# Performance work log

Hardware: AMD Instinct MI355X
Metric: run time of the kernel (lower is better)

## Reference

```python
import jax, jax.numpy as jnp
import numpy as np


def _forward(embed, enc_Wih, enc_Whh, enc_bih, enc_bhh,
             dec_Wih, dec_Whh, dec_bih, dec_bhh,
             qk_W, qk_b, qv_W, qv_b, ak_W, ak_b,
             out_W, out_b, wd_b,
             hfc1_W, hfc1_b, hfc2_W, hfc2_b,
             cfc1_W, cfc1_b, cfc2_W, cfc2_b,
             src_seqs, src_lengths, trg_seqs):
    B, S = src_seqs.shape
    H = enc_Whh.shape[1]

    # ---- encoder LSTM over packed (masked) source ----
    src_embed = embed[src_seqs]                      # [B,S,D]
    xs = jnp.swapaxes(src_embed, 0, 1)               # [S,B,D]
    step_mask = jnp.arange(S)[:, None] < src_lengths[None, :]  # [S,B]

    def enc_step(carry, inp):
        h, c = carry
        x, m = inp
        z = x @ enc_Wih.T + enc_bih + h @ enc_Whh.T + enc_bhh
        i, f, g, o = jnp.split(z, 4, axis=-1)
        c_new = jax.nn.sigmoid(f) * c + jax.nn.sigmoid(i) * jnp.tanh(g)
        h_new = jax.nn.sigmoid(o) * jnp.tanh(c_new)
        m = m[:, None]
        h_new = jnp.where(m, h_new, h)
        c_new = jnp.where(m, c_new, c)
        out = jnp.where(m, h_new, 0.0)               # pad_packed zero-fills
        return (h_new, c_new), out

    h0 = jnp.zeros((B, H), embed.dtype)
    (hT, cT), enc_outs = jax.lax.scan(enc_step, (h0, h0), (xs, step_mask))
    src_hidden = jnp.swapaxes(enc_outs, 0, 1)        # [B,S,H]

    # ---- init_hidden: MLP transforms of final encoder state ----
    dh = jax.nn.relu(hT @ hfc1_W.T + hfc1_b) @ hfc2_W.T + hfc2_b
    dc = jax.nn.relu(cT @ cfc1_W.T + cfc1_b) @ cfc2_W.T + cfc2_b

    # ---- attention keys/values (constant across decode steps) ----
    q_key = jnp.tanh(src_hidden @ qk_W.T + qk_b)     # [B,S,K]
    q_value = src_hidden @ qv_W.T + qv_b             # [B,S,H]
    attn_mask = jnp.arange(S)[None, :] < src_lengths[:, None]  # [B,S]

    # ---- teacher-forced decode loop (sampling_rate = 1.0) ----
    ans_embed = embed[trg_seqs]                      # [B,T,D]
    dec_inputs = jnp.swapaxes(ans_embed[:, :-1, :], 0, 1)  # [T-1,B,D]

    def dec_step(carry, x):
        h, c = carry
        a_key = jnp.tanh(h @ ak_W.T + ak_b)          # [B,K]
        energy = jnp.einsum('bsk,bk->bs', q_key, a_key)
        energy = jnp.where(attn_mask, energy, -jnp.inf)
        w = jax.nn.softmax(energy, axis=1)           # [B,S]
        context = jnp.einsum('bs,bsh->bh', w, q_value)
        xin = jnp.concatenate([x, context], axis=1)  # [B,D+H]
        z = xin @ dec_Wih.T + dec_bih + h @ dec_Whh.T + dec_bhh
        i, f, g, o = jnp.split(z, 4, axis=-1)
        c_new = jax.nn.sigmoid(f) * c + jax.nn.sigmoid(i) * jnp.tanh(g)
        h_new = jax.nn.sigmoid(o) * jnp.tanh(c_new)
        feat = jnp.concatenate([h_new, context], axis=1) @ out_W.T + out_b  # [B,D]
        logits = feat @ embed.T + wd_b               # tied word_dist, [B,V]
        return (h_new, c_new), logits

    _, outs = jax.lax.scan(dec_step, (dh, dc), dec_inputs)  # [T-1,B,V]
    return jnp.swapaxes(outs, 0, 1)                  # [B,T-1,V]


def setup_inputs() -> dict:
    key = jax.random.key(0)
    ks = jax.random.split(key, 30)
    V, D, H, K = 32000, 512, 1024, 100
    B, S, T = 32, 128, 20

    def w(k, shape):
        return jax.random.normal(k, shape, jnp.float32) * 0.05

    inp = {
        'embed': w(ks[0], (V, D)).at[0].set(0.0),  # padding_idx = 0
        'enc_Wih': w(ks[1], (4 * H, D)), 'enc_Whh': w(ks[2], (4 * H, H)),
        'enc_bih': w(ks[3], (4 * H,)).at[H:2 * H].set(0.0),
        'enc_bhh': w(ks[4], (4 * H,)).at[H:2 * H].set(0.0),
        'dec_Wih': w(ks[5], (4 * H, D + H)), 'dec_Whh': w(ks[6], (4 * H, H)),
        'dec_bih': w(ks[7], (4 * H,)).at[H:2 * H].set(0.0),
        'dec_bhh': w(ks[8], (4 * H,)).at[H:2 * H].set(0.0),
        'qk_W': w(ks[9], (K, H)), 'qk_b': w(ks[10], (K,)),
        'qv_W': w(ks[11], (H, H)), 'qv_b': w(ks[12], (H,)),
        'ak_W': w(ks[13], (K, H)), 'ak_b': w(ks[14], (K,)),
        'out_W': w(ks[15], (D, 2 * H)), 'out_b': w(ks[16], (D,)),
        'wd_b': w(ks[17], (V,)),
        'hfc1_W': w(ks[18], (2 * H, H)), 'hfc1_b': w(ks[19], (2 * H,)),
        'hfc2_W': w(ks[20], (H, 2 * H)), 'hfc2_b': w(ks[21], (H,)),
        'cfc1_W': w(ks[22], (2 * H, H)), 'cfc1_b': w(ks[23], (2 * H,)),
        'cfc2_W': w(ks[24], (H, 2 * H)), 'cfc2_b': w(ks[25], (H,)),
    }
    inp['src_seqs'] = jax.random.randint(ks[26], (B, S), 1, V)
    lens = jnp.sort(jax.random.randint(ks[27], (B,), 1, S + 1))[::-1]
    inp['src_lengths'] = lens.at[0].set(S)  # sorted descending, max = S
    inp['trg_seqs'] = jax.random.randint(ks[28], (B, T), 1, V)
    return inp


def reference(embed, enc_Wih, enc_Whh, enc_bih, enc_bhh,
              dec_Wih, dec_Whh, dec_bih, dec_bhh,
              qk_W, qk_b, qv_W, qv_b, ak_W, ak_b,
              out_W, out_b, wd_b,
              hfc1_W, hfc1_b, hfc2_W, hfc2_b,
              cfc1_W, cfc1_b, cfc2_W, cfc2_b,
              src_seqs, src_lengths, trg_seqs):
    return _forward(embed, enc_Wih, enc_Whh, enc_bih, enc_bhh,
                    dec_Wih, dec_Whh, dec_bih, dec_bhh,
                    qk_W, qk_b, qv_W, qv_b, ak_W, ak_b,
                    out_W, out_b, wd_b,
                    hfc1_W, hfc1_b, hfc2_W, hfc2_b,
                    cfc1_W, cfc1_b, cfc2_W, cfc2_b,
                    src_seqs, src_lengths, trg_seqs)
```

## Files before the change

kernel.cpp:

```cpp
#include <hip/hip_runtime.h>
#include <hip/hip_bf16.h>


using bf16 = __hip_bfloat16;
typedef __attribute__((ext_vector_type(8))) __bf16 bf16x8;
typedef __attribute__((ext_vector_type(4))) float f32x4;

__device__ __forceinline__ bf16x8 ld8(const bf16* p) {
    return *reinterpret_cast<const bf16x8*>(p);
}
__device__ __forceinline__ float b2f(bf16 v) { return __bfloat162float(v); }
__device__ __forceinline__ bf16 f2b(float v) { return __float2bfloat16(v); }
__device__ __forceinline__ unsigned short b2u(bf16 v) {
    unsigned short u; __builtin_memcpy(&u, &v, 2); return u;
}
__device__ __forceinline__ float sigf(float x) { return 1.0f / (1.0f + expf(-x)); }

#define MFMA(a, b, c) __builtin_amdgcn_mfma_f32_16x16x32_bf16((a), (b), (c), 0, 0, 0)

struct ConvDesc { const float* src; bf16* dst; int n; };
struct ConvTable { ConvDesc d[13]; };

__global__ __launch_bounds__(256) void k_conv(ConvTable tab) {
    ConvDesc cd = tab.d[blockIdx.y];
    int stride = gridDim.x * blockDim.x * 4;
    for (int i = (blockIdx.x * blockDim.x + threadIdx.x) * 4; i < cd.n; i += stride) {
        float4 v = *reinterpret_cast<const float4*>(cd.src + i);
        bf16 tmp[4] = {f2b(v.x), f2b(v.y), f2b(v.z), f2b(v.w)};
        *reinterpret_cast<ushort4*>(cd.dst + i) = *reinterpret_cast<const ushort4*>(tmp);
    }
}

__global__ __launch_bounds__(256) void k_gather(const unsigned int* __restrict__ table,
                                                const int* __restrict__ idx,
                                                unsigned int* __restrict__ out) {
    int r = blockIdx.x;
    out[(size_t)r * 256 + threadIdx.x] = table[(size_t)idx[r] * 256 + threadIdx.x];
}

__global__ __launch_bounds__(256) void k_gemm_bt(const bf16* __restrict__ A,
                                                 const bf16* __restrict__ Bw,
                                                 const float* __restrict__ bias,
                                                 float* __restrict__ outF,
                                                 bf16* __restrict__ outB,
                                                 int M, int N, int K, int ldo,
                                                 int ntN, int mode, int xcdmap) {
    int bx = blockIdx.x;
    int mt, nt;
    if (xcdmap) {
        int ntM = (M + 127) >> 7;
        int x = bx & 7, w = bx >> 3;
        mt = w % ntM;
        nt = (w / ntM) * 8 + x;
        if (nt >= ntN) return;
    } else {
        mt = bx / ntN;
        nt = bx % ntN;
    }
    int tid = threadIdx.x, wv = tid >> 6, l = tid & 63;
    int m0 = mt * 128 + (wv >> 1) * 64;
    int n0 = nt * 128 + (wv & 1) * 64;
    int r = l & 15, ko = (l >> 4) * 8;

    const bf16* ap[4];
    const bf16* bp[4];
#pragma unroll
    for (int i = 0; i < 4; ++i) {
        int row = m0 + i * 16 + r;
        if (row > M - 1) row = M - 1;
        ap[i] = A + (size_t)row * K + ko;
    }
#pragma unroll
    for (int j = 0; j < 4; ++j) {
        int n = n0 + j * 16 + r;
        if (n > N - 1) n = N - 1;
        bp[j] = Bw + (size_t)n * K + ko;
    }

    f32x4 zv = {0.f, 0.f, 0.f, 0.f};
    f32x4 acc[4][4];
#pragma unroll
    for (int i = 0; i < 4; ++i)
#pragma unroll
        for (int j = 0; j < 4; ++j) acc[i][j] = zv;

    int nk = K >> 5;
    for (int kk = 0; kk < nk; ++kk) {
        bf16x8 af[4], bfv[4];
#pragma unroll
        for (int i = 0; i < 4; ++i) af[i] = ld8(ap[i] + kk * 32);
#pragma unroll
        for (int j = 0; j < 4; ++j) bfv[j] = ld8(bp[j] + kk * 32);
#pragma unroll
        for (int i = 0; i < 4; ++i)
#pragma unroll
            for (int j = 0; j < 4; ++j) acc[i][j] = MFMA(af[i], bfv[j], acc[i][j]);
    }

    int ccol = l & 15, cr = (l >> 4) * 4;
#pragma unroll
    for (int i = 0; i < 4; ++i) {
#pragma unroll
        for (int j = 0; j < 4; ++j) {
            int n = n0 + j * 16 + ccol;
            if (n >= N) continue;
            float bv = bias ? bias[n] : 0.f;
#pragma unroll
            for (int q = 0; q < 4; ++q) {
                int row = m0 + i * 16 + cr + q;
                if (row >= M) continue;
                float v = acc[i][j][q] + bv;
                if (mode == 1) v = tanhf(v);
                if (mode == 2) {
                    outF[((size_t)(row & 31) * 19 + (size_t)(row >> 5)) * 32000 + n] = v;
                } else if (mode == 3) {
                    outB[(size_t)row * ldo + n] = f2b(v);
                } else {
                    outF[(size_t)row * ldo + n] = v;
                }
            }
        }
    }
}

__global__ __launch_bounds__(64) void k_gemm_sm(const bf16* __restrict__ A,
                                                const bf16* __restrict__ W,
                                                const float* __restrict__ bias,
                                                float* __restrict__ outF, int ldof,
                                                bf16* __restrict__ outB, int ldob,
                                                int K, int ntN, int act) {
    int bx = blockIdx.x;
    int mt = bx / ntN, nt = bx % ntN;
    int l = threadIdx.x;
    int r = l & 15, ko = (l >> 4) * 8;
    const bf16* ap = A + (size_t)(mt * 16 + r) * K + ko;
    const bf16* bp = W + (size_t)(nt * 16 + r) * K + ko;
    f32x4 acc = {0.f, 0.f, 0.f, 0.f};
    int nk = K >> 5;
#pragma unroll 4
    for (int kk = 0; kk < nk; ++kk) acc = MFMA(ld8(ap + kk * 32), ld8(bp + kk * 32), acc);
    int n = nt * 16 + (l & 15);
    int cr = (l >> 4) * 4;
    float bv = bias ? bias[n] : 0.f;
#pragma unroll
    for (int q = 0; q < 4; ++q) {
        int row = mt * 16 + cr + q;
        float v = acc[q] + bv;
        if (act == 1) v = fmaxf(v, 0.f);
        if (act == 2) v = tanhf(v);
        if (outF) outF[(size_t)row * ldof + n] = v;
        if (outB) outB[(size_t)row * ldob + n] = f2b(v);
    }
}

__global__ __launch_bounds__(256, 1) void k_enc_all(const bf16* __restrict__ Zx,
                                                    const bf16* __restrict__ Whh,
                                                    const float* __restrict__ bih,
                                                    const float* __restrict__ bhh,
                                                    const int* __restrict__ lens,
                                                    unsigned int* __restrict__ hbw0,
                                                    unsigned int* __restrict__ hbw1,
                                                    bf16* __restrict__ cbT,
                                                    bf16* __restrict__ SH,
                                                    int* __restrict__ flags) {
    __shared__ bf16 hlds[8][1024];
    __shared__ float zl[4][8][16];
    __shared__ unsigned short hpub[8][16];
    unsigned int* hldsw = (unsigned int*)hlds;
    const bf16x8* hldsv = (const bf16x8*)hlds;

    int bid = blockIdx.x;
    int grp = bid >> 6, jblk = bid & 63;
    int j0 = jblk * 16;
    int tid = threadIdx.x;
    int g = tid >> 6, l = tid & 63;
    int r = l & 15, ko = (l >> 4) * 8;

    bf16x8 wreg[32];
    {
        const bf16* wp = Whh + (size_t)(g * 1024 + j0 + r) * 1024 + ko;
#pragma unroll
        for (int kk = 0; kk < 32; ++kk) wreg[kk] = ld8(wp + kk * 32);
    }

    int bl = tid >> 4, ji = tid & 15;
    int b = grp * 8 + bl;
    int j = j0 + ji;
    bool pw = tid < 128;
    float bs[4] = {0.f, 0.f, 0.f, 0.f};
    int lenv = 0;
    float hs = 0.f, cs = 0.f;
    const bf16* zxp = Zx;
    if (pw) {
#pragma unroll
        for (int gg = 0; gg < 4; ++gg) bs[gg] = bih[gg * 1024 + j] + bhh[gg * 1024 + j];
        lenv = lens[b];
        zxp = Zx + (size_t)(b * 128) * 4096 + j;
    }
    int ccol = l & 15, cr = (l >> 4) * 4;
    int rk = r & 7;
    unsigned int gbase = grp * 4096;

    for (int t = 0; t < 128; ++t) {
        float za[4] = {0.f, 0.f, 0.f, 0.f};
        if (pw) {
#pragma unroll
            for (int gg = 0; gg < 4; ++gg)
                za[gg] = b2f(zxp[(size_t)t * 4096 + gg * 1024]);
        }

        if (t > 0) {
            if (tid < 64) {
                const int* fp = flags + (t - 1) * 256 + grp * 64;
                while (true) {
                    int v = __hip_atomic_load(fp + l, __ATOMIC_RELAXED,
                                              __HIP_MEMORY_SCOPE_AGENT);
                    if (__all(v != 0)) break;
                    __builtin_amdgcn_s_sleep(1);
                }
                __builtin_amdgcn_sched_barrier(0);
            }
            __syncthreads();
        }

        const unsigned int* hw = ((t & 1) ? hbw1 : hbw0) + gbase;
#pragma unroll 4
        for (int i = 0; i < 16; ++i) {
            int d = i * 256 + tid;
            int bb = d >> 9, w = d & 511;
            unsigned int v = __hip_atomic_load(hw + d, __ATOMIC_RELAXED,
                                               __HIP_MEMORY_SCOPE_AGENT);
            hldsw[bb * 512 + ((((w >> 2) ^ (bb & 7)) << 2) | (w & 3))] = v;
        }
        __syncthreads();

        f32x4 acc0 = {0.f, 0.f, 0.f, 0.f};
#pragma unroll
        for (int kk = 0; kk < 32; ++kk) {
            int u = kk * 4 + (l >> 4);
            acc0 = MFMA(hldsv[(r & 7) * 128 + (u ^ rk)], wreg[kk], acc0);
        }
        if (l < 32) {
#pragma unroll
            for (int q = 0; q < 4; ++q) zl[g][cr + q][ccol] = acc0[q];
        }
        __syncthreads();

        if (pw) {
            float zi = zl[0][bl][ji] + za[0] + bs[0];
            float zf = zl[1][bl][ji] + za[1] + bs[1];
            float zg = zl[2][bl][ji] + za[2] + bs[2];
            float zo = zl[3][bl][ji] + za[3] + bs[3];
            float cn = sigf(zf) * cs + sigf(zi) * tanhf(zg);
            float hn = sigf(zo) * tanhf(cn);
            bool msk = t < lenv;
            if (msk) { hs = hn; cs = cn; }
            hpub[bl][ji] = b2u(f2b(hs));
            SH[((size_t)b * 128 + t) * 1024 + j] = msk ? f2b(hn) : f2b(0.f);
            if (t == 127) cbT[b * 1024 + j] = f2b(cs);
        }
        __syncthreads();

        unsigned int* hwn = ((t & 1) ? hbw0 : hbw1) + gbase;
        if (tid < 64) {
            int pb = tid >> 3, pq = tid & 7;
            unsigned int val = (unsigned int)hpub[pb][2 * pq] |
                               ((unsigned int)hpub[pb][2 * pq + 1] << 16);
            __hip_atomic_store(hwn + (size_t)pb * 512 + (j0 >> 1) + pq, val,
                               __ATOMIC_RELAXED, __HIP_MEMORY_SCOPE_AGENT);
        }
        __syncthreads();
        if (tid == 0)
            __hip_atomic_fetch_add(flags + t * 256 + grp * 64 + jblk, 1,
                                   __ATOMIC_RELAXED, __HIP_MEMORY_SCOPE_AGENT);
    }
}

__global__ __launch_bounds__(256) void k_attn(const bf16* __restrict__ embedB,
                                              const int* __restrict__ trg,
                                              const bf16* __restrict__ akWB,
                                              const float* __restrict__ akb,
                                              const float* __restrict__ qkB,
                                              const bf16* __restrict__ qvBb,
                                              const int* __restrict__ lens,
                                              const bf16* __restrict__ hb,
                                              bf16* __restrict__ xin,
                                              bf16* __restrict__ featT, int t) {
    int b = blockIdx.x >> 2, chunk = blockIdx.x & 3;
    int tid = threadIdx.x;
    if (chunk == 0) {
        const unsigned int* er = (const unsigned int*)(embedB + (size_t)trg[b * 20 + t] * 512);
        ((unsigned int*)(xin + (size_t)b * 1536))[tid] = er[tid];
    }

    __shared__ float part[256];
    __shared__ float ak[100];
    __shared__ float ew[128];
    __shared__ float mxs, inv_s;

    float s = 0.f;
    if (tid < 200) {
        int n = tid >> 1, hh = tid & 1;
        const bf16* wr = akWB + (size_t)n * 1024 + hh * 512;
        const bf16* hr = hb + (size_t)b * 1024 + hh * 512;
#pragma unroll 8
        for (int k = 0; k < 512; ++k) s += b2f(hr[k]) * b2f(wr[k]);
    }
    part[tid] = s;
    __syncthreads();
    if (tid < 100) ak[tid] = tanhf(part[2 * tid] + part[2 * tid + 1] + akb[tid]);
    __syncthreads();

    if (tid < 128) {
        const float* qr = qkB + ((size_t)b * 128 + tid) * 100;
        float e = 0.f;
#pragma unroll 4
        for (int k = 0; k < 100; ++k) e += qr[k] * ak[k];
        ew[tid] = (tid < lens[b]) ? e : -INFINITY;
    }
    __syncthreads();
    if (tid < 64) {
        float m = fmaxf(ew[tid], ew[tid + 64]);
#pragma unroll
        for (int off = 32; off; off >>= 1) m = fmaxf(m, __shfl_down(m, off));
        if (tid == 0) mxs = m;
    }
    __syncthreads();
    if (tid < 128) ew[tid] = expf(ew[tid] - mxs);
    __syncthreads();
    if (tid < 64) {
        float s2 = ew[tid] + ew[tid + 64];
#pragma unroll
        for (int off = 32; off; off >>= 1) s2 += __shfl_down(s2, off);
        if (tid == 0) inv_s = 1.0f / s2;
    }
    __syncthreads();

    {
        int jj = (chunk << 8) + tid;
        const bf16* qvb = qvBb + ((size_t)b * 128) * 1024 + jj;
        float a0 = 0.f;
#pragma unroll 4
        for (int s3 = 0; s3 < 128; ++s3) a0 += ew[s3] * b2f(qvb[(size_t)s3 * 1024]);
        a0 *= inv_s;
        bf16 cb = f2b(a0);
        xin[(size_t)b * 1536 + 512 + jj] = cb;
        featT[(size_t)b * 2048 + 1024 + jj] = cb;
    }
}

__global__ __launch_bounds__(64) void k_dec_z(const bf16* __restrict__ xin,
                                              const bf16* __restrict__ Wih,
                                              const bf16* __restrict__ hb_in,
                                              const bf16* __restrict__ Whh,
                                              const float* __restrict__ bih,
                                              const float* __restrict__ bhh,
                                              float* __restrict__ cd,
                                              bf16* __restrict__ hb_out,
                                              bf16* __restrict__ featT) {
    __shared__ float zl[32][16];
    int j0 = blockIdx.x * 4;
    int l = threadIdx.x;
    int r = l & 15, ko = (l >> 4) * 8;
    int wrow = (r >> 2) * 1024 + j0 + (r & 3);

    f32x4 acc0 = {0.f, 0.f, 0.f, 0.f}, acc1 = {0.f, 0.f, 0.f, 0.f};
    {
        const bf16* a0 = xin + (size_t)r * 1536 + ko;
        const bf16* a1 = xin + (size_t)(16 + r) * 1536 + ko;
        const bf16* bp = Wih + (size_t)wrow * 1536 + ko;
#pragma unroll 4
        for (int kk = 0; kk < 48; ++kk) {
            bf16x8 bv = ld8(bp + kk * 32);
            acc0 = MFMA(ld8(a0 + kk * 32), bv, acc0);
            acc1 = MFMA(ld8(a1 + kk * 32), bv, acc1);
        }
    }
    {
        const bf16* a0 = hb_in + (size_t)r * 1024 + ko;
        const bf16* a1 = hb_in + (size_t)(16 + r) * 1024 + ko;
        const bf16* bp = Whh + (size_t)wrow * 1024 + ko;
#pragma unroll 4
        for (int kk = 0; kk < 32; ++kk) {
            bf16x8 bv = ld8(bp + kk * 32);
            acc0 = MFMA(ld8(a0 + kk * 32), bv, acc0);
            acc1 = MFMA(ld8(a1 + kk * 32), bv, acc1);
        }
    }
    int ccol = l & 15, cr = (l >> 4) * 4;
#pragma unroll
    for (int q = 0; q < 4; ++q) {
        zl[cr + q][ccol] = acc0[q];
        zl[16 + cr + q][ccol] = acc1[q];
    }
    __syncthreads();

#pragma unroll
    for (int e = l; e < 128; e += 64) {
        int b = e >> 2, jj = e & 3;
        int j = j0 + jj;
        float zi = zl[b][jj]      + bih[j]        + bhh[j];
        float zf = zl[b][4 + jj]  + bih[1024 + j] + bhh[1024 + j];
        float zg = zl[b][8 + jj]  + bih[2048 + j] + bhh[2048 + j];
        float zo = zl[b][12 + jj] + bih[3072 + j] + bhh[3072 + j];
        int hi = b * 1024 + j;
        float co = cd[hi];
        float cn = sigf(zf) * co + sigf(zi) * tanhf(zg);
        float hn = sigf(zo) * tanhf(cn);
        cd[hi] = cn;
        bf16 hnb = f2b(hn);
        hb_out[hi] = hnb;
        featT[(size_t)b * 2048 + j] = hnb;
    }
}

extern "C" void kernel_launch(void* const* d_in, const int* in_sizes, int n_in,
                              void* d_out, int out_size, void* d_ws, size_t ws_size,
                              hipStream_t stream) {
    const float* embed   = (const float*)d_in[0];
    const float* enc_Wih = (const float*)d_in[1];
    const float* enc_Whh = (const float*)d_in[2];
    const float* enc_bih = (const float*)d_in[3];
    const float* enc_bhh = (const float*)d_in[4];
    const float* dec_Wih = (const float*)d_in[5];
    const float* dec_Whh = (const float*)d_in[6];
    const float* dec_bih = (const float*)d_in[7];
    const float* dec_bhh = (const float*)d_in[8];
    const float* qk_W    = (const float*)d_in[9];
    const float* qk_b    = (const float*)d_in[10];
    const float* qv_W    = (const float*)d_in[11];
    const float* qv_b    = (const float*)d_in[12];
    const float* ak_W    = (const float*)d_in[13];
    const float* ak_b    = (const float*)d_in[14];
    const float* out_W   = (const float*)d_in[15];
    const float* out_b   = (const float*)d_in[16];
    const float* wd_b    = (const float*)d_in[17];
    const float* hfc1_W  = (const float*)d_in[18];
    const float* hfc1_b  = (const float*)d_in[19];
    const float* hfc2_W  = (const float*)d_in[20];
    const float* hfc2_b  = (const float*)d_in[21];
    const float* cfc1_W  = (const float*)d_in[22];
    const float* cfc1_b  = (const float*)d_in[23];
    const float* cfc2_W  = (const float*)d_in[24];
    const float* cfc2_b  = (const float*)d_in[25];
    const int* src  = (const int*)d_in[26];
    const int* lens = (const int*)d_in[27];
    const int* trg  = (const int*)d_in[28];

    char* cur = (char*)d_ws;
    auto alloc = [&](size_t bytes) -> char* {
        char* p = cur;
        cur += (bytes + 255) & ~(size_t)255;
        return p;
    };
    bf16* embedB  = (bf16*)alloc((size_t)16384000 * 2);
    bf16* encWihB = (bf16*)alloc((size_t)2097152 * 2);
    bf16* encWhhB = (bf16*)alloc((size_t)4194304 * 2);
    bf16* decWihB = (bf16*)alloc((size_t)6291456 * 2);
    bf16* decWhhB = (bf16*)alloc((size_t)4194304 * 2);
    bf16* qkWB    = (bf16*)alloc((size_t)102400 * 2);
    bf16* qvWB    = (bf16*)alloc((size_t)1048576 * 2);
    bf16* outWB   = (bf16*)alloc((size_t)1048576 * 2);
    bf16* hfc1B   = (bf16*)alloc((size_t)2097152 * 2);
    bf16* hfc2B   = (bf16*)alloc((size_t)2097152 * 2);
    bf16* cfc1B   = (bf16*)alloc((size_t)2097152 * 2);
    bf16* cfc2B   = (bf16*)alloc((size_t)2097152 * 2);
    bf16* akWB    = (bf16*)alloc((size_t)102400 * 2);
    bf16*  Xsrc  = (bf16*)alloc((size_t)4096 * 512 * 2);
    bf16*  Zx    = (bf16*)alloc((size_t)4096 * 4096 * 2);
    bf16*  SH    = (bf16*)alloc((size_t)4096 * 1024 * 2);
    float* qkB   = (float*)alloc((size_t)4096 * 100 * 4);
    bf16*  qvBb  = (bf16*)alloc((size_t)4096 * 1024 * 2);
    bf16*  hbA   = (bf16*)alloc(32 * 1024 * 2);
    bf16*  hbB   = (bf16*)alloc(32 * 1024 * 2);
    bf16*  cbT   = (bf16*)alloc(32 * 1024 * 2);
    bf16*  t1    = (bf16*)alloc(32 * 2048 * 2);
    float* cd    = (float*)alloc(32 * 1024 * 4);
    bf16*  hdA   = (bf16*)alloc(32 * 1024 * 2);
    bf16*  hdB   = (bf16*)alloc(32 * 1024 * 2);
    bf16*  xin   = (bf16*)alloc(32 * 1536 * 2);
    bf16*  featAll = (bf16*)alloc((size_t)608 * 2048 * 2);
    bf16*  feats = (bf16*)alloc((size_t)608 * 512 * 2);
    int*   flags = (int*)alloc((size_t)128 * 256 * 4);
    if ((size_t)(cur - (char*)d_ws) > ws_size) return;

    hipMemsetAsync(hbA, 0, 32 * 1024 * 2, stream);
    hipMemsetAsync(flags, 0, (size_t)128 * 256 * 4, stream);

    ConvTable tab;
    tab.d[0]  = {embed,   embedB,  16384000};
    tab.d[1]  = {enc_Wih, encWihB, 2097152};
    tab.d[2]  = {enc_Whh, encWhhB, 4194304};
    tab.d[3]  = {dec_Wih, decWihB, 6291456};
    tab.d[4]  = {dec_Whh, decWhhB, 4194304};
    tab.d[5]  = {qk_W,    qkWB,    102400};
    tab.d[6]  = {qv_W,    qvWB,    1048576};
    tab.d[7]  = {out_W,   outWB,   1048576};
    tab.d[8]  = {hfc1_W,  hfc1B,   2097152};
    tab.d[9]  = {hfc2_W,  hfc2B,   2097152};
    tab.d[10] = {cfc1_W,  cfc1B,   2097152};
    tab.d[11] = {cfc2_W,  cfc2B,   2097152};
    tab.d[12] = {ak_W,    akWB,    102400};
    k_conv<<<dim3(1024, 13), 256, 0, stream>>>(tab);

    k_gather<<<4096, 256, 0, stream>>>((const unsigned int*)embedB, src, (unsigned int*)Xsrc);

    k_gemm_bt<<<32 * 32, 256, 0, stream>>>(Xsrc, encWihB, nullptr, nullptr, Zx,
                                           4096, 4096, 512, 4096, 32, 3, 0);

    {
        const bf16* ZxA = Zx;  const bf16* WhhA = encWhhB;
        const float* bihA = enc_bih; const float* bhhA = enc_bhh;
        const int* lensA = lens;
        unsigned int* hb0A = (unsigned int*)hbA;
        unsigned int* hb1A = (unsigned int*)hbB;
        bf16* cbTA = cbT; bf16* SHA = SH; int* flagsA = flags;
        void* args[] = {(void*)&ZxA, (void*)&WhhA, (void*)&bihA, (void*)&bhhA,
                        (void*)&lensA, (void*)&hb0A, (void*)&hb1A, (void*)&cbTA,
                        (void*)&SHA, (void*)&flagsA};
        hipLaunchCooperativeKernel((void*)k_enc_all, dim3(256), dim3(256), args, 0, stream);
    }
    bf16* hbT = hbA;

    k_gemm_sm<<<256, 64, 0, stream>>>(hbT, hfc1B, hfc1_b, nullptr, 0, t1, 2048, 1024, 128, 1);
    k_gemm_sm<<<128, 64, 0, stream>>>(t1, hfc2B, hfc2_b, nullptr, 0, hdA, 1024, 2048, 64, 0);
    k_gemm_sm<<<256, 64, 0, stream>>>(cbT, cfc1B, cfc1_b, nullptr, 0, t1, 2048, 1024, 128, 1);
    k_gemm_sm<<<128, 64, 0, stream>>>(t1, cfc2B, cfc2_b, cd, 1024, nullptr, 0, 2048, 64, 0);

    k_gemm_bt<<<32, 256, 0, stream>>>(SH, qkWB, qk_b, qkB, nullptr,
                                      4096, 100, 1024, 100, 1, 1, 0);
    k_gemm_bt<<<256, 256, 0, stream>>>(SH, qvWB, qv_b, nullptr, qvBb,
                                       4096, 1024, 1024, 1024, 8, 3, 0);

    for (int t = 0; t < 19; ++t) {
        const bf16* hin = (t & 1) ? hdB : hdA;
        bf16* hout = (t & 1) ? hdA : hdB;
        bf16* featT = featAll + (size_t)t * 32 * 2048;
        k_attn<<<128, 256, 0, stream>>>(embedB, trg, akWB, ak_b, qkB, qvBb, lens,
                                        hin, xin, featT, t);
        k_dec_z<<<256, 64, 0, stream>>>(xin, decWihB, hin, decWhhB, dec_bih, dec_bhh,
                                        cd, hout, featT);
    }

    k_gemm_bt<<<20, 256, 0, stream>>>(featAll, outWB, out_b, nullptr, feats,
                                      608, 512, 2048, 512, 4, 3, 0);

    k_gemm_bt<<<1280, 256, 0, stream>>>(feats, embedB, wd_b, (float*)d_out, nullptr,
                                        608, 32000, 512, 0, 250, 2, 1);
}
```

Baseline: 2.158 ms.

## Stage GEMM tiles in LDS via direct global-to-LDS loads with XOR swizzle

The tiled GEMM kernel now cooperatively loads 128x32 A and B tiles into shared memory with global_load_lds, using an XOR swizzle on 16-byte chunks, then each wave reads its MFMA fragments from LDS. Before, each wave loaded its operands straight from global memory, so tiles shared by waves were fetched twice. The goal is less redundant global/L2 traffic. In exchange the loop gains two barriers per K step and has no double-buffering, which may expose load latency.

```diff
diff --git a/kernel.cpp b/kernel.cpp
--- a/kernel.cpp
+++ b/kernel.cpp
@@ -17,6 +17,12 @@
 __device__ __forceinline__ float sigf(float x) { return 1.0f / (1.0f + expf(-x)); }
 
 #define MFMA(a, b, c) __builtin_amdgcn_mfma_f32_16x16x32_bf16((a), (b), (c), 0, 0, 0)
+
+__device__ __forceinline__ void gload_lds16(const bf16* g, bf16* l) {
+    __builtin_amdgcn_global_load_lds(
+        (const __attribute__((address_space(1))) void*)g,
+        (__attribute__((address_space(3))) void*)l, 16, 0, 0);
+}
 
 struct ConvDesc { const float* src; bf16* dst; int n; };
 struct ConvTable { ConvDesc d[13]; };
@@ -45,6 +51,9 @@
                                                  bf16* __restrict__ outB,
                                                  int M, int N, int K, int ldo,
                                                  int ntN, int mode, int xcdmap) {
+    __shared__ __attribute__((aligned(16))) bf16 ldsA[128 * 32];
+    __shared__ __attribute__((aligned(16))) bf16 ldsB[128 * 32];
+
     int bx = blockIdx.x;
     int mt, nt;
     if (xcdmap) {
@@ -58,24 +67,12 @@
         nt = bx % ntN;
     }
     int tid = threadIdx.x, wv = tid >> 6, l = tid & 63;
-    int m0 = mt * 128 + (wv >> 1) * 64;
-    int n0 = nt * 128 + (wv & 1) * 64;
-    int r = l & 15, ko = (l >> 4) * 8;
-
-    const bf16* ap[4];
-    const bf16* bp[4];
-#pragma unroll
-    for (int i = 0; i < 4; ++i) {
-        int row = m0 + i * 16 + r;
-        if (row > M - 1) row = M - 1;
-        ap[i] = A + (size_t)row * K + ko;
-    }
-#pragma unroll
-    for (int j = 0; j < 4; ++j) {
-        int n = n0 + j * 16 + r;
-        if (n > N - 1) n = N - 1;
-        bp[j] = Bw + (size_t)n * K + ko;
-    }
+    int m0 = mt * 128, n0 = nt * 128;
+    int m0w = (wv >> 1) * 64;
+    int n0w = (wv & 1) * 64;
+    int r = l & 15, ko = l >> 4;
+
+    int srow0 = (l >> 2), suc = l & 3;
 
     f32x4 zv = {0.f, 0.f, 0.f, 0.f};
     f32x4 acc[4][4];
@@ -84,13 +81,34 @@
 #pragma unroll
         for (int j = 0; j < 4; ++j) acc[i][j] = zv;
 
-    int nk = K >> 5;
-    for (int kk = 0; kk < nk; ++kk) {
+    const bf16x8* LA = (const bf16x8*)ldsA;
+    const bf16x8* LB = (const bf16x8*)ldsB;
+
+    for (int kk = 0; kk < K; kk += 32) {
+        __syncthreads();
+#pragma unroll
+        for (int c = 0; c < 2; ++c) {
+            int rbase = c * 64 + wv * 16;
+            int row = rbase + srow0;
+            int gcu = (suc ^ (row & 3)) << 3;
+            int arow = m0 + row; if (arow > M - 1) arow = M - 1;
+            int brow = n0 + row; if (brow > N - 1) brow = N - 1;
+            gload_lds16(A + (size_t)arow * K + kk + gcu, ldsA + rbase * 32);
+            gload_lds16(Bw + (size_t)brow * K + kk + gcu, ldsB + rbase * 32);
+        }
+        __syncthreads();
+
         bf16x8 af[4], bfv[4];
 #pragma unroll
-        for (int i = 0; i < 4; ++i) af[i] = ld8(ap[i] + kk * 32);
-#pragma unroll
-        for (int j = 0; j < 4; ++j) bfv[j] = ld8(bp[j] + kk * 32);
+        for (int i = 0; i < 4; ++i) {
+            int row = m0w + i * 16 + r;
+            af[i] = LA[row * 4 + (ko ^ (row & 3))];
+        }
+#pragma unroll
+        for (int j = 0; j < 4; ++j) {
+            int row = n0w + j * 16 + r;
+            bfv[j] = LB[row * 4 + (ko ^ (row & 3))];
+        }
 #pragma unroll
         for (int i = 0; i < 4; ++i)
 #pragma unroll
@@ -102,12 +120,12 @@
     for (int i = 0; i < 4; ++i) {
 #pragma unroll
         for (int j = 0; j < 4; ++j) {
-            int n = n0 + j * 16 + ccol;
+            int n = n0 + n0w + j * 16 + ccol;
             if (n >= N) continue;
             float bv = bias ? bias[n] : 0.f;
 #pragma unroll
             for (int q = 0; q < 4; ++q) {
-                int row = m0 + i * 16 + cr + q;
+                int row = m0 + m0w + i * 16 + cr + q;
                 if (row >= M) continue;
                 float v = acc[i][j][q] + bv;
                 if (mode == 1) v = tanhf(v);
```

New measurement: 2.051 ms. -4.9%, faster.
